# Kernel optimization log

Measured on AMD Instinct MI355X. Metric: run time of the kernel, lower is better.

Reference implementation:

```python
import jax, jax.numpy as jnp
import numpy as np

DIM = 768
NUM_HEADS = 12
HEAD_DIM = DIM // NUM_HEADS
SCALE = HEAD_DIM ** -0.5


def setup_inputs() -> dict:
    key = jax.random.key(0)
    k1, k2, k3 = jax.random.split(key, 3)
    x = jax.random.normal(k1, (32, 577, DIM), dtype=jnp.float32)
    # torch nn.Linear weights are [out_features, in_features]
    W_qkv = jax.random.normal(k2, (3 * DIM, DIM), dtype=jnp.float32) * (DIM ** -0.5)
    W_proj = jax.random.normal(k3, (DIM, DIM), dtype=jnp.float32) * (DIM ** -0.5)
    b_proj = jnp.zeros((DIM,), dtype=jnp.float32)
    return {"x": x, "W_qkv": W_qkv, "W_proj": W_proj, "b_proj": b_proj}


def reference(x, W_qkv, W_proj, b_proj):
    B, N, C = x.shape
    H, D = NUM_HEADS, C // NUM_HEADS
    # qkv: [B, N, 3C] -> [3, B, H, N, D]
    qkv = (x @ W_qkv.T).reshape(B, N, 3, H, D).transpose(2, 0, 3, 1, 4)
    q, k, v = qkv[0], qkv[1], qkv[2]
    attn = jnp.einsum('bhnd,bhmd->bhnm', q, k) * SCALE
    attn = jax.nn.softmax(attn, axis=-1)
    out = jnp.einsum('bhnm,bhmd->bhnd', attn, v)  # [B, H, N, D]
    out = out.transpose(0, 2, 1, 3).reshape(B, N, C)
    return out @ W_proj.T + b_proj
```

## Files before the change

### kernel.cpp

```cpp
#include <hip/hip_runtime.h>
#include <math.h>

#define SEQ    577
#define BATCH  32
#define DIM    768
#define NHEAD  12
#define HDIM   64
#define MROWS  (BATCH * SEQ)
#define QKVN   (3 * DIM)

using half4   = __attribute__((ext_vector_type(4))) _Float16;
using half8   = __attribute__((ext_vector_type(8))) _Float16;
using floatx4 = __attribute__((ext_vector_type(4))) float;

typedef __attribute__((address_space(1))) const unsigned int GU;
typedef __attribute__((address_space(3))) unsigned int LU;

__device__ __forceinline__ void gld_lds16(const _Float16* g, _Float16* l) {
    __builtin_amdgcn_global_load_lds((const GU*)g, (LU*)l, 16, 0, 0);
}

__global__ void cvt3_f32_f16(const float* __restrict__ a, _Float16* __restrict__ ao, int na4,
                             const float* __restrict__ b, _Float16* __restrict__ bo, int nb4,
                             const float* __restrict__ c, _Float16* __restrict__ co, int nc4)
{
    int i = blockIdx.x * blockDim.x + threadIdx.x;
    int stride = gridDim.x * blockDim.x;
    int total = na4 + nb4 + nc4;
    for (; i < total; i += stride) {
        const float4* src; half4* dst; int j = i;
        if (j < na4)            { src = (const float4*)a; dst = (half4*)ao; }
        else if ((j -= na4) < nb4) { src = (const float4*)b; dst = (half4*)bo; }
        else { j -= nb4;          src = (const float4*)c; dst = (half4*)co; }
        float4 v = src[j];
        half4 h;
        h[0] = (_Float16)v.x; h[1] = (_Float16)v.y;
        h[2] = (_Float16)v.z; h[3] = (_Float16)v.w;
        dst[j] = h;
    }
}

template<int OUT_HALF, int HAS_BIAS>
__global__ __launch_bounds__(256) void gemm_f16_lds(
    const _Float16* __restrict__ A, const _Float16* __restrict__ B,
    const float* __restrict__ bias, void* __restrict__ Cp,
    int M, int N, int K, int npm, int npn)
{
    __shared__ _Float16 As[2][128 * 32];
    __shared__ _Float16 Bs[2][128 * 32];

    const int GROUP = 8;
    int pid  = blockIdx.x;
    int ngrp = GROUP * npn;
    int g    = pid / ngrp;
    int fm   = g * GROUP;
    int gm   = npm - fm; if (gm > GROUP) gm = GROUP;
    int pm   = fm + (pid % ngrp) % gm;
    int pn   = (pid % ngrp) / gm;
    const int m0 = pm * 128, n0 = pn * 128;

    const int t    = threadIdx.x, lane = t & 63, wv = t >> 6;
    const int quad = lane >> 4,   ln   = lane & 15;
    const int wm   = wv >> 1,     wn   = wv & 1;

    floatx4 acc[4][4];
#pragma unroll
    for (int mt = 0; mt < 4; mt++)
#pragma unroll
        for (int nt = 0; nt < 4; nt++) acc[mt][nt] = {0.f, 0.f, 0.f, 0.f};

    const int sr = wv * 32 + (lane >> 2);
    const int sc = (lane & 3) * 8;
    int ma0 = m0 + sr;      if (ma0 > M - 1) ma0 = M - 1;
    int ma1 = m0 + sr + 16; if (ma1 > M - 1) ma1 = M - 1;
    const _Float16* Ag0 = A + (size_t)ma0 * K + sc;
    const _Float16* Ag1 = A + (size_t)ma1 * K + sc;
    const _Float16* Bg0 = B + (size_t)(n0 + sr) * K + sc;
    const _Float16* Bg1 = B + (size_t)(n0 + sr + 16) * K + sc;
    _Float16* Al0 = &As[0][sr * 32 + sc];
    _Float16* Al1 = &As[0][(sr + 16) * 32 + sc];
    _Float16* Bl0 = &Bs[0][sr * 32 + sc];
    _Float16* Bl1 = &Bs[0][(sr + 16) * 32 + sc];
    const int PHALF = 128 * 32;

    for (int k0 = 0; k0 < K; k0 += 64) {
        __syncthreads();
#pragma unroll
        for (int p = 0; p < 2; p++) {
            gld_lds16(Ag0 + k0 + p * 32, Al0 + p * PHALF);
            gld_lds16(Ag1 + k0 + p * 32, Al1 + p * PHALF);
            gld_lds16(Bg0 + k0 + p * 32, Bl0 + p * PHALF);
            gld_lds16(Bg1 + k0 + p * 32, Bl1 + p * PHALF);
        }
        __syncthreads();

#pragma unroll
        for (int p = 0; p < 2; p++) {
            half8 af[4], bf[4];
#pragma unroll
            for (int mt = 0; mt < 4; mt++)
                af[mt] = *(const half8*)&As[p][(wm * 64 + mt * 16 + ln) * 32 + quad * 8];
#pragma unroll
            for (int nt = 0; nt < 4; nt++)
                bf[nt] = *(const half8*)&Bs[p][(wn * 64 + nt * 16 + ln) * 32 + quad * 8];
#pragma unroll
            for (int mt = 0; mt < 4; mt++)
#pragma unroll
                for (int nt = 0; nt < 4; nt++)
                    acc[mt][nt] = __builtin_amdgcn_mfma_f32_16x16x32_f16(
                        af[mt], bf[nt], acc[mt][nt], 0, 0, 0);
        }
    }

    float bv[4];
    if constexpr (HAS_BIAS) {
#pragma unroll
        for (int nt = 0; nt < 4; nt++) bv[nt] = bias[n0 + wn * 64 + nt * 16 + ln];
    }
    float*    C32 = (float*)Cp;
    _Float16* C16 = (_Float16*)Cp;
#pragma unroll
    for (int mt = 0; mt < 4; mt++)
#pragma unroll
        for (int r = 0; r < 4; r++) {
            int m = m0 + wm * 64 + mt * 16 + quad * 4 + r;
            if (m < M) {
#pragma unroll
                for (int nt = 0; nt < 4; nt++) {
                    int col = n0 + wn * 64 + nt * 16 + ln;
                    float v = acc[mt][nt][r];
                    if constexpr (HAS_BIAS) v += bv[nt];
                    if constexpr (OUT_HALF) C16[(size_t)m * N + col] = (_Float16)v;
                    else                    C32[(size_t)m * N + col] = v;
                }
            }
        }
}

__global__ __launch_bounds__(256) void attn_f16(
    const _Float16* __restrict__ qkv, _Float16* __restrict__ outp)
{
    constexpr int LK = 72, LV = 68;
    __shared__ _Float16 Ks[64 * LK];
    __shared__ _Float16 Vs[64 * LV];

    const int t    = threadIdx.x, lane = t & 63, wv = t >> 6;
    const int quad = lane >> 4,   ln   = lane & 15;
    const int q0   = blockIdx.x * 128;
    const int hd   = blockIdx.y,  b    = blockIdx.z;
    const _Float16* base = qkv + (size_t)b * SEQ * QKVN;

    half8 qreg[2][2];
#pragma unroll
    for (int qc = 0; qc < 2; qc++) {
        int q = q0 + wv * 32 + qc * 16 + ln; if (q >= SEQ) q = SEQ - 1;
#pragma unroll
        for (int kd = 0; kd < 2; kd++)
            qreg[qc][kd] = *(const half8*)(base + (size_t)q * QKVN + hd * HDIM + kd * 32 + quad * 8);
    }

    const float CL = 0.125f * 1.44269504f;
    float lr[2] = {0.f, 0.f};
    floatx4 o[2][4];
#pragma unroll
    for (int qc = 0; qc < 2; qc++)
#pragma unroll
        for (int dt = 0; dt < 4; dt++) o[qc][dt] = {0.f, 0.f, 0.f, 0.f};

    for (int kt0 = 0; kt0 < 10; kt0++) {
        const int k0 = kt0 * 64;

        uint4 krg[2], vrg[2];
#pragma unroll
        for (int i = 0; i < 2; i++) {
            int idx = t + (i << 8);
            int key = idx >> 3, dc = idx & 7;
            int n = k0 + key; if (n >= SEQ) n = SEQ - 1;
            const _Float16* p = base + (size_t)n * QKVN + DIM + hd * HDIM + dc * 8;
            krg[i] = *(const uint4*)p;
            vrg[i] = *(const uint4*)(p + DIM);
        }
        __syncthreads();
#pragma unroll
        for (int i = 0; i < 2; i++) {
            int idx = t + (i << 8);
            int key = idx >> 3, dc = idx & 7;
            *(uint4*)&Ks[key * LK + dc * 8] = krg[i];
            const unsigned short* vh = (const unsigned short*)&vrg[i];
            unsigned short* vs = (unsigned short*)Vs;
#pragma unroll
            for (int j = 0; j < 8; j++)
                vs[(dc * 8 + j) * LV + key] = vh[j];
        }
        __syncthreads();

        floatx4 sacc[2][4];
#pragma unroll
        for (int qc = 0; qc < 2; qc++)
#pragma unroll
            for (int mt = 0; mt < 4; mt++) sacc[qc][mt] = {0.f, 0.f, 0.f, 0.f};
#pragma unroll
        for (int kd = 0; kd < 2; kd++) {
            half8 kf[4];
#pragma unroll
            for (int mt = 0; mt < 4; mt++)
                kf[mt] = *(const half8*)&Ks[(mt * 16 + ln) * LK + kd * 32 + quad * 8];
#pragma unroll
            for (int mt = 0; mt < 4; mt++) {
                sacc[0][mt] = __builtin_amdgcn_mfma_f32_16x16x32_f16(kf[mt], qreg[0][kd], sacc[0][mt], 0, 0, 0);
                sacc[1][mt] = __builtin_amdgcn_mfma_f32_16x16x32_f16(kf[mt], qreg[1][kd], sacc[1][mt], 0, 0, 0);
            }
        }

        if (k0 + 64 > SEQ) {
#pragma unroll
            for (int mt = 0; mt < 4; mt++)
#pragma unroll
                for (int r = 0; r < 4; r++)
                    if (k0 + mt * 16 + quad * 4 + r >= SEQ) {
                        sacc[0][mt][r] = -3e38f;
                        sacc[1][mt][r] = -3e38f;
                    }
        }

        half4 pf[2][4];
#pragma unroll
        for (int qc = 0; qc < 2; qc++) {
            float ls = 0.f;
#pragma unroll
            for (int mt = 0; mt < 4; mt++)
#pragma unroll
                for (int r = 0; r < 4; r++) {
                    float p = exp2f(sacc[qc][mt][r] * CL);
                    ls += p;
                    pf[qc][mt][r] = (_Float16)p;
                }
            ls += __shfl_xor(ls, 16);
            ls += __shfl_xor(ls, 32);
            lr[qc] += ls;
        }

#pragma unroll
        for (int kt = 0; kt < 4; kt++)
#pragma unroll
            for (int dt = 0; dt < 4; dt++) {
                half4 vf = *(const half4*)&Vs[(dt * 16 + ln) * LV + kt * 16 + quad * 4];
                o[0][dt] = __builtin_amdgcn_mfma_f32_16x16x16f16(vf, pf[0][kt], o[0][dt], 0, 0, 0);
                o[1][dt] = __builtin_amdgcn_mfma_f32_16x16x16f16(vf, pf[1][kt], o[1][dt], 0, 0, 0);
            }
    }

#pragma unroll
    for (int qc = 0; qc < 2; qc++) {
        int q = q0 + wv * 32 + qc * 16 + ln;
        if (q < SEQ) {
            float inv = 1.f / lr[qc];
#pragma unroll
            for (int dt = 0; dt < 4; dt++) {
                half4 hv;
                hv[0] = (_Float16)(o[qc][dt][0] * inv);
                hv[1] = (_Float16)(o[qc][dt][1] * inv);
                hv[2] = (_Float16)(o[qc][dt][2] * inv);
                hv[3] = (_Float16)(o[qc][dt][3] * inv);
                *(half4*)&outp[(size_t)(b * SEQ + q) * DIM + hd * HDIM + dt * 16 + quad * 4] = hv;
            }
        }
    }
}

extern "C" void kernel_launch(void* const* d_in, const int* in_sizes, int n_in,
                              void* d_out, int out_size, void* d_ws, size_t ws_size,
                              hipStream_t stream)
{
    const float* x     = (const float*)d_in[0];
    const float* Wqkv  = (const float*)d_in[1];
    const float* Wproj = (const float*)d_in[2];
    const float* bproj = (const float*)d_in[3];
    float* out = (float*)d_out;

    const size_t NX  = (size_t)MROWS * DIM;
    const size_t NWQ = (size_t)QKVN * DIM;
    const size_t NWP = (size_t)DIM * DIM;

    _Float16* x16    = (_Float16*)d_ws;
    _Float16* Wq16   = x16 + NX;
    _Float16* Wp16   = Wq16 + NWQ;
    _Float16* qkv16  = Wp16 + NWP;
    _Float16* attn16 = qkv16 + (size_t)MROWS * QKVN;

    cvt3_f32_f16<<<2048, 256, 0, stream>>>(x, x16, (int)(NX / 4),
                                           Wqkv, Wq16, (int)(NWQ / 4),
                                           Wproj, Wp16, (int)(NWP / 4));

    {
        int npm = (MROWS + 127) / 128, npn = QKVN / 128;
        gemm_f16_lds<1, 0><<<npm * npn, 256, 0, stream>>>(
            x16, Wq16, nullptr, qkv16, MROWS, QKVN, DIM, npm, npn);
    }

    attn_f16<<<dim3((SEQ + 127) / 128, NHEAD, BATCH), 256, 0, stream>>>(qkv16, attn16);

    {
        int npm = (MROWS + 127) / 128, npn = DIM / 128;
        gemm_f16_lds<0, 1><<<npm * npn, 256, 0, stream>>>(
            attn16, Wp16, bproj, out, MROWS, DIM, DIM, npm, npn);
    }
}
```

Before: 359.2 us.

## Swizzle K tile, use transposed LDS reads for V, fold softmax scale into Q

The K tile in LDS now uses an XOR-swizzled, unpadded layout. V is stored in a pre-permuted layout and read with ds_read_b64_tr_b16 transposed loads, which replaces the scalar 16-bit scatter stores used to transpose V. The softmax scale times log2(e) is folded into the Q columns at the QKV GEMM epilogue, so the attention kernel skips one multiply per score. Costs are inline asm with explicit waitcnt and sched barriers that constrain scheduling, and Q is rounded to fp16 after scaling.

Result: slower. 415.3 us (+15.6%).

```diff
diff --git a/kernel.cpp b/kernel.cpp
--- a/kernel.cpp
+++ b/kernel.cpp
@@ -18,6 +18,10 @@
 
 __device__ __forceinline__ void gld_lds16(const _Float16* g, _Float16* l) {
     __builtin_amdgcn_global_load_lds((const GU*)g, (LU*)l, 16, 0, 0);
+}
+
+__device__ __forceinline__ unsigned lds_addr(const void* p) {
+    return (unsigned)(size_t)(LU*)p;
 }
 
 __global__ void cvt3_f32_f16(const float* __restrict__ a, _Float16* __restrict__ ao, int na4,
@@ -40,7 +44,7 @@
     }
 }
 
-template<int OUT_HALF, int HAS_BIAS>
+template<int OUT_HALF, int HAS_BIAS, int SCALEQ>
 __global__ __launch_bounds__(256) void gemm_f16_lds(
     const _Float16* __restrict__ A, const _Float16* __restrict__ B,
     const float* __restrict__ bias, void* __restrict__ Cp,
@@ -130,6 +134,7 @@
                     int col = n0 + wn * 64 + nt * 16 + ln;
                     float v = acc[mt][nt][r];
                     if constexpr (HAS_BIAS) v += bv[nt];
+                    if constexpr (SCALEQ) { if (col < DIM) v *= 0.18033688f; }
                     if constexpr (OUT_HALF) C16[(size_t)m * N + col] = (_Float16)v;
                     else                    C32[(size_t)m * N + col] = v;
                 }
@@ -140,9 +145,8 @@
 __global__ __launch_bounds__(256) void attn_f16(
     const _Float16* __restrict__ qkv, _Float16* __restrict__ outp)
 {
-    constexpr int LK = 72, LV = 68;
-    __shared__ _Float16 Ks[64 * LK];
-    __shared__ _Float16 Vs[64 * LV];
+    __shared__ _Float16 Ks[64 * 64];
+    __shared__ _Float16 Vs[64 * 64];
 
     const int t    = threadIdx.x, lane = t & 63, wv = t >> 6;
     const int quad = lane >> 4,   ln   = lane & 15;
@@ -159,7 +163,6 @@
             qreg[qc][kd] = *(const half8*)(base + (size_t)q * QKVN + hd * HDIM + kd * 32 + quad * 8);
     }
 
-    const float CL = 0.125f * 1.44269504f;
     float lr[2] = {0.f, 0.f};
     floatx4 o[2][4];
 #pragma unroll
@@ -167,30 +170,29 @@
 #pragma unroll
         for (int dt = 0; dt < 4; dt++) o[qc][dt] = {0.f, 0.f, 0.f, 0.f};
 
+    const unsigned vb = lds_addr(Vs) + lane * 8;
+
     for (int kt0 = 0; kt0 < 10; kt0++) {
         const int k0 = kt0 * 64;
 
         uint4 krg[2], vrg[2];
 #pragma unroll
         for (int i = 0; i < 2; i++) {
-            int idx = t + (i << 8);
-            int key = idx >> 3, dc = idx & 7;
-            int n = k0 + key; if (n >= SEQ) n = SEQ - 1;
-            const _Float16* p = base + (size_t)n * QKVN + DIM + hd * HDIM + dc * 8;
-            krg[i] = *(const uint4*)p;
-            vrg[i] = *(const uint4*)(p + DIM);
+            int C = t + (i << 8);
+            int krow = C >> 3, kdc = (C & 7) ^ (krow & 7);
+            int nk = k0 + krow; if (nk >= SEQ) nk = SEQ - 1;
+            krg[i] = *(const uint4*)(base + (size_t)nk * QKVN + DIM + hd * HDIM + kdc * 8);
+            int vkey = ((C >> 7) << 4) + (((C >> 3) & 3) << 2) + ((C >> 1) & 3);
+            int vd0  = (((C >> 5) & 3) << 4) + ((C & 1) << 3);
+            int nv = k0 + vkey; if (nv >= SEQ) nv = SEQ - 1;
+            vrg[i] = *(const uint4*)(base + (size_t)nv * QKVN + 2 * DIM + hd * HDIM + vd0);
         }
         __syncthreads();
 #pragma unroll
         for (int i = 0; i < 2; i++) {
-            int idx = t + (i << 8);
-            int key = idx >> 3, dc = idx & 7;
-            *(uint4*)&Ks[key * LK + dc * 8] = krg[i];
-            const unsigned short* vh = (const unsigned short*)&vrg[i];
-            unsigned short* vs = (unsigned short*)Vs;
-#pragma unroll
-            for (int j = 0; j < 8; j++)
-                vs[(dc * 8 + j) * LV + key] = vh[j];
+            int C = t + (i << 8);
+            *(uint4*)&Ks[C << 3] = krg[i];
+            *(uint4*)&Vs[C << 3] = vrg[i];
         }
         __syncthreads();
 
@@ -199,12 +201,13 @@
         for (int qc = 0; qc < 2; qc++)
 #pragma unroll
             for (int mt = 0; mt < 4; mt++) sacc[qc][mt] = {0.f, 0.f, 0.f, 0.f};
+        const int xr = ln & 7;
 #pragma unroll
         for (int kd = 0; kd < 2; kd++) {
             half8 kf[4];
 #pragma unroll
             for (int mt = 0; mt < 4; mt++)
-                kf[mt] = *(const half8*)&Ks[(mt * 16 + ln) * LK + kd * 32 + quad * 8];
+                kf[mt] = *(const half8*)&Ks[(mt * 16 + ln) * 64 + (((kd * 4 + quad) ^ xr) << 3)];
 #pragma unroll
             for (int mt = 0; mt < 4; mt++) {
                 sacc[0][mt] = __builtin_amdgcn_mfma_f32_16x16x32_f16(kf[mt], qreg[0][kd], sacc[0][mt], 0, 0, 0);
@@ -231,7 +234,7 @@
             for (int mt = 0; mt < 4; mt++)
 #pragma unroll
                 for (int r = 0; r < 4; r++) {
-                    float p = exp2f(sacc[qc][mt][r] * CL);
+                    float p = exp2f(sacc[qc][mt][r]);
                     ls += p;
                     pf[qc][mt][r] = (_Float16)p;
                 }
@@ -241,13 +244,24 @@
         }
 
 #pragma unroll
-        for (int kt = 0; kt < 4; kt++)
-#pragma unroll
-            for (int dt = 0; dt < 4; dt++) {
-                half4 vf = *(const half4*)&Vs[(dt * 16 + ln) * LV + kt * 16 + quad * 4];
-                o[0][dt] = __builtin_amdgcn_mfma_f32_16x16x16f16(vf, pf[0][kt], o[0][dt], 0, 0, 0);
-                o[1][dt] = __builtin_amdgcn_mfma_f32_16x16x16f16(vf, pf[1][kt], o[1][dt], 0, 0, 0);
-            }
+        for (int kt = 0; kt < 4; kt++) {
+            half4 vf0, vf1, vf2, vf3;
+            unsigned a = vb + kt * 2048;
+            asm volatile("ds_read_b64_tr_b16 %0, %1 offset:0"    : "=v"(vf0) : "v"(a));
+            asm volatile("ds_read_b64_tr_b16 %0, %1 offset:512"  : "=v"(vf1) : "v"(a));
+            asm volatile("ds_read_b64_tr_b16 %0, %1 offset:1024" : "=v"(vf2) : "v"(a));
+            asm volatile("ds_read_b64_tr_b16 %0, %1 offset:1536" : "=v"(vf3) : "v"(a));
+            asm volatile("s_waitcnt lgkmcnt(0)" ::: "memory");
+            __builtin_amdgcn_sched_barrier(0);
+            o[0][0] = __builtin_amdgcn_mfma_f32_16x16x16f16(vf0, pf[0][kt], o[0][0], 0, 0, 0);
+            o[1][0] = __builtin_amdgcn_mfma_f32_16x16x16f16(vf0, pf[1][kt], o[1][0], 0, 0, 0);
+            o[0][1] = __builtin_amdgcn_mfma_f32_16x16x16f16(vf1, pf[0][kt], o[0][1], 0, 0, 0);
+            o[1][1] = __builtin_amdgcn_mfma_f32_16x16x16f16(vf1, pf[1][kt], o[1][1], 0, 0, 0);
+            o[0][2] = __builtin_amdgcn_mfma_f32_16x16x16f16(vf2, pf[0][kt], o[0][2], 0, 0, 0);
+            o[1][2] = __builtin_amdgcn_mfma_f32_16x16x16f16(vf2, pf[1][kt], o[1][2], 0, 0, 0);
+            o[0][3] = __builtin_amdgcn_mfma_f32_16x16x16f16(vf3, pf[0][kt], o[0][3], 0, 0, 0);
+            o[1][3] = __builtin_amdgcn_mfma_f32_16x16x16f16(vf3, pf[1][kt], o[1][3], 0, 0, 0);
+        }
     }
 
 #pragma unroll
@@ -294,7 +308,7 @@
 
     {
         int npm = (MROWS + 127) / 128, npn = QKVN / 128;
-        gemm_f16_lds<1, 0><<<npm * npn, 256, 0, stream>>>(
+        gemm_f16_lds<1, 0, 1><<<npm * npn, 256, 0, stream>>>(
             x16, Wq16, nullptr, qkv16, MROWS, QKVN, DIM, npm, npn);
     }
 
@@ -302,7 +316,7 @@
 
     {
         int npm = (MROWS + 127) / 128, npn = DIM / 128;
-        gemm_f16_lds<0, 1><<<npm * npn, 256, 0, stream>>>(
+        gemm_f16_lds<0, 1, 0><<<npm * npn, 256, 0, stream>>>(
             attn16, Wp16, bproj, out, MROWS, DIM, DIM, npm, npn);
     }
 }
```
